# Optimization experiments

Hardware: AMD Instinct MI355X
Metric: run time of the kernel (lower is better)

Reference implementation:

```python
import jax, jax.numpy as jnp
import numpy as np

N = 100000
IN_C = 128
HID = 128
LAT = 64
E = 800000


def gcn_conv(x, src, dst, norm, W, b, num_nodes):
    # x: [N, Cin]; src/dst: [E+N] (self-loops appended); norm: [E+N]
    xw = x @ W                                   # [N, Cout]
    msg = xw[src] * norm[:, None]                # gather + scale, [E+N, Cout]
    out = jax.ops.segment_sum(msg, dst, num_segments=num_nodes)
    return out + b


def setup_inputs() -> dict:
    key = jax.random.key(0)
    ks = jax.random.split(key, 8)
    x = jax.random.normal(ks[0], (N, IN_C), dtype=jnp.float32)
    edge_index = jax.random.randint(ks[1], (2, E), 0, N, dtype=jnp.int64)
    batch = jnp.zeros((N,), dtype=jnp.int64)
    # GCNConv params (Glorot-ish scale)
    W1 = jax.random.normal(ks[2], (IN_C, HID), dtype=jnp.float32) / np.sqrt(IN_C)
    b1 = jnp.zeros((HID,), dtype=jnp.float32)
    Wmu = jax.random.normal(ks[3], (HID, LAT), dtype=jnp.float32) / np.sqrt(HID)
    bmu = jnp.zeros((LAT,), dtype=jnp.float32)
    Wlv = jax.random.normal(ks[4], (HID, LAT), dtype=jnp.float32) / np.sqrt(HID)
    blv = jnp.zeros((LAT,), dtype=jnp.float32)
    return {"x": x, "edge_index": edge_index, "batch": batch,
            "W1": W1, "b1": b1, "Wmu": Wmu, "bmu": bmu, "Wlv": Wlv, "blv": blv}


def reference(x, edge_index, batch, W1, b1, Wmu, bmu, Wlv, blv):
    num_nodes = x.shape[0]
    loop = jnp.arange(num_nodes, dtype=edge_index.dtype)
    src = jnp.concatenate([edge_index[0], loop])   # source nodes (+self loops)
    dst = jnp.concatenate([edge_index[1], loop])   # target nodes (+self loops)
    # symmetric GCN normalization: deg over targets, norm = d[src]^-1/2 * d[dst]^-1/2
    deg = jax.ops.segment_sum(jnp.ones_like(dst, dtype=x.dtype), dst,
                              num_segments=num_nodes)
    dis = jnp.where(deg > 0, jax.lax.rsqrt(deg), 0.0)
    norm = dis[src] * dis[dst]                      # [E+N]

    h = jax.nn.relu(gcn_conv(x, src, dst, norm, W1, b1, num_nodes))
    mu = gcn_conv(h, src, dst, norm, Wmu, bmu, num_nodes)
    logvar = gcn_conv(h, src, dst, norm, Wlv, blv, num_nodes)
    return (mu, logvar)
```

## Files before the change

kernel.cpp:

```cpp
#include <hip/hip_runtime.h>

typedef short bf16x8 __attribute__((ext_vector_type(8)));
typedef float f32x4 __attribute__((ext_vector_type(4)));

#define ELLK 32
#define OCAP 4096
#define CSTRIDE 16

static __device__ __forceinline__ float4 f4zero() { return make_float4(0.f, 0.f, 0.f, 0.f); }

static __device__ __forceinline__ unsigned short f2bf(float f) {
  unsigned u = __float_as_uint(f);
  u += 0x7FFFu + ((u >> 16) & 1u);
  return (unsigned short)(u >> 16);
}
static __device__ __forceinline__ float2 bf2x2(unsigned u) {
  float2 r;
  r.x = __uint_as_float(u << 16);
  r.y = __uint_as_float(u & 0xFFFF0000u);
  return r;
}

__global__ void k_setup(const float* __restrict__ W1, const float* __restrict__ Wmu,
                        const float* __restrict__ Wlv, unsigned short* __restrict__ Wt1,
                        unsigned short* __restrict__ Wt2, uint4* __restrict__ cntz,
                        int* __restrict__ ocount, int nz4, int nbz) {
  int b = blockIdx.x;
  if (b < nbz) {
    int i = b * 256 + threadIdx.x;
    if (i < nz4) cntz[i] = make_uint4(0u, 0u, 0u, 0u);
    if (b == 0 && threadIdx.x == 0) *ocount = 0;
  } else {
    int id = (b - nbz) * 256 + threadIdx.x;
    if (id < 16384) {
      int nn = id >> 7, k = id & 127;
      Wt1[id] = f2bf(W1[k * 128 + nn]);
    } else {
      int id2 = id - 16384;
      int nn = id2 >> 7, k = id2 & 127;
      float v = (nn < 64) ? Wmu[k * 64 + nn] : Wlv[k * 64 + (nn - 64)];
      Wt2[id2] = f2bf(v);
    }
  }
}

__global__ void k_fill(const int* __restrict__ ei, int* __restrict__ cnt,
                       int* __restrict__ ell, int2* __restrict__ ovf,
                       int* __restrict__ ocount, int E, int n) {
  int e = blockIdx.x * 256 + threadIdx.x;
  if (e >= E) return;
  int s = ei[e];
  int d = ei[E + e];
  int pos = atomicAdd(&cnt[(size_t)d * CSTRIDE], 1);
  if (pos < ELLK) {
    ell[(size_t)pos * n + d] = s;
  } else {
    int o = atomicAdd(ocount, 1);
    if (o < OCAP) ovf[o] = make_int2(d, s);
  }
}

__global__ void k_dnorm(const int* __restrict__ cnt, float* __restrict__ dnorm,
                        unsigned* __restrict__ mflag, unsigned* __restrict__ A,
                        unsigned* __restrict__ H, int n) {
  if (blockIdx.x == 0 && threadIdx.x < 128) {
    int t = threadIdx.x;
    if (t < 64) A[(size_t)n * 64 + t] = 0u;
    else        H[(size_t)n * 64 + (t - 64)] = 0u;
  }
  int i = blockIdx.x * 256 + threadIdx.x;
  if (i >= n) return;
  int c = cnt[(size_t)i * CSTRIDE];
  dnorm[i] = rsqrtf((float)(c + 1));
  int m = (c < ELLK) ? c : ELLK;
  mflag[i] = (unsigned)m | ((c > ELLK) ? 0x80000000u : 0u);
}

__global__ __launch_bounds__(256) void k_gemm1(
    const float* __restrict__ x, const unsigned short* __restrict__ Wt,
    const float* __restrict__ dnorm, unsigned short* __restrict__ A, int n) {
  __shared__ unsigned short Wl[128 * 136];
  __shared__ unsigned short Xl[64 * 136];
  const int tid = threadIdx.x;
  const int row0 = blockIdx.x * 64;
  {
    const uint4* Wg = (const uint4*)Wt;
#pragma unroll
    for (int i = 0; i < 8; ++i) {
      int idx = tid + i * 256;
      int r = idx >> 4, c = idx & 15;
      *(uint4*)&Wl[r * 136 + c * 8] = Wg[r * 16 + c];
    }
  }
  {
#pragma unroll
    for (int i = 0; i < 8; ++i) {
      int idx = tid + i * 256;
      int r = idx >> 5, c = idx & 31;
      int gi = row0 + r;
      float4 v = (gi < n) ? ((const float4*)x)[(size_t)gi * 32 + c] : f4zero();
      ushort4 p;
      p.x = f2bf(v.x); p.y = f2bf(v.y); p.z = f2bf(v.z); p.w = f2bf(v.w);
      *(ushort4*)&Xl[r * 136 + c * 4] = p;
    }
  }
  __syncthreads();

  const int wave = tid >> 6, lane = tid & 63;
  const int li = lane & 15, quad = lane >> 4;
  const int m0 = wave * 16;
  f32x4 acc[8];
#pragma unroll
  for (int t = 0; t < 8; ++t) acc[t] = (f32x4){0.f, 0.f, 0.f, 0.f};

#pragma unroll
  for (int kk = 0; kk < 4; ++kk) {
    int ko = kk * 32 + quad * 8;
    bf16x8 a = *(const bf16x8*)&Xl[(m0 + li) * 136 + ko];
#pragma unroll
    for (int nt = 0; nt < 8; ++nt) {
      bf16x8 b = *(const bf16x8*)&Wl[(nt * 16 + li) * 136 + ko];
      acc[nt] = __builtin_amdgcn_mfma_f32_16x16x32_bf16(a, b, acc[nt], 0, 0, 0);
    }
  }
  float dn[4];
#pragma unroll
  for (int r = 0; r < 4; ++r) {
    int gi = row0 + m0 + quad * 4 + r;
    dn[r] = (gi < n) ? dnorm[gi] : 0.f;
  }
  __syncthreads();
#pragma unroll
  for (int nt = 0; nt < 8; ++nt)
#pragma unroll
    for (int r = 0; r < 4; ++r)
      Xl[(m0 + quad * 4 + r) * 136 + nt * 16 + li] = f2bf(acc[nt][r] * dn[r]);
  __syncthreads();
  {
    uint4* A4 = (uint4*)A;
#pragma unroll
    for (int i = 0; i < 4; ++i) {
      int idx = tid + i * 256;
      int r = idx >> 4, c = idx & 15;
      int gi = row0 + r;
      if (gi < n) A4[(size_t)gi * 16 + c] = *(uint4*)&Xl[r * 136 + c * 8];
    }
  }
}

template <bool EPI_RELU>
__global__ __launch_bounds__(256) void k_spmm(
    const unsigned* __restrict__ mflag, const float* __restrict__ dnorm,
    const int* __restrict__ ell, const int2* __restrict__ ovf,
    const int* __restrict__ ocount, const unsigned* __restrict__ S,
    unsigned* __restrict__ D, const float2* __restrict__ bias, int n) {
  int wid = (blockIdx.x * blockDim.x + threadIdx.x) >> 6;
  if (wid >= n) return;
  int lane = threadIdx.x & 63;

  unsigned mf = mflag[wid];
  int m = (int)(mf & 0xFFFFu);
  float dsd = dnorm[wid];
  float2 acc = bf2x2(S[(size_t)wid * 64 + lane]);

  const int* ep = ell + wid;
  int nbt = (m + 7) >> 3;
  for (int b = 0; b < nbt; ++b) {
    int j0 = b * 8;
    int idx[8];
#pragma unroll
    for (int k = 0; k < 8; ++k) idx[k] = ep[(size_t)(j0 + k) * n];
#pragma unroll
    for (int k = 0; k < 8; ++k) idx[k] = (j0 + k < m) ? idx[k] : n;
    unsigned u[8];
#pragma unroll
    for (int k = 0; k < 8; ++k) u[k] = S[(size_t)idx[k] * 64 + lane];
#pragma unroll
    for (int k = 0; k < 8; ++k) {
      float2 f = bf2x2(u[k]);
      acc.x += f.x;
      acc.y += f.y;
    }
  }
  if (mf & 0x80000000u) {
    int oc = *ocount;
    if (oc > OCAP) oc = OCAP;
    for (int k = 0; k < oc; ++k) {
      int2 e = ovf[k];
      if (e.x == wid) {
        float2 u0 = bf2x2(S[(size_t)e.y * 64 + lane]);
        acc.x += u0.x;
        acc.y += u0.y;
      }
    }
  }
  float2 o;
  if (EPI_RELU) {
    float2 b = bias[lane];
    o.x = dsd * fmaxf(fmaf(dsd, acc.x, b.x), 0.f);
    o.y = dsd * fmaxf(fmaf(dsd, acc.y, b.y), 0.f);
  } else {
    o.x = dsd * acc.x;
    o.y = dsd * acc.y;
  }
  unsigned pk = (unsigned)f2bf(o.x) | ((unsigned)f2bf(o.y) << 16);
  D[(size_t)wid * 64 + lane] = pk;
}

__global__ __launch_bounds__(256) void k_gemm2_mfma(
    const unsigned short* __restrict__ G, const unsigned short* __restrict__ Wt,
    const float* __restrict__ bmu, const float* __restrict__ blv,
    float* __restrict__ out, int n) {
  __shared__ unsigned short Wl[128 * 136];
  __shared__ unsigned short Xl[64 * 136];
  const int tid = threadIdx.x;
  const int row0 = blockIdx.x * 64;
  {
    const uint4* Wg = (const uint4*)Wt;
#pragma unroll
    for (int i = 0; i < 8; ++i) {
      int idx = tid + i * 256;
      int r = idx >> 4, c = idx & 15;
      *(uint4*)&Wl[r * 136 + c * 8] = Wg[r * 16 + c];
    }
  }
  {
    const uint4* Gg = (const uint4*)G;
#pragma unroll
    for (int i = 0; i < 4; ++i) {
      int idx = tid + i * 256;
      int r = idx >> 4, c = idx & 15;
      int gi = row0 + r;
      uint4 v = (gi < n) ? Gg[(size_t)gi * 16 + c] : make_uint4(0, 0, 0, 0);
      *(uint4*)&Xl[r * 136 + c * 8] = v;
    }
  }
  __syncthreads();

  const int wave = tid >> 6, lane = tid & 63;
  const int li = lane & 15, quad = lane >> 4;
  const int m0 = wave * 16;

  float bias[8];
#pragma unroll
  for (int nt = 0; nt < 8; ++nt) {
    int c = nt * 16 + li;
    bias[nt] = (c < 64) ? bmu[c] : blv[c - 64];
  }

  f32x4 acc[8];
#pragma unroll
  for (int t = 0; t < 8; ++t) acc[t] = (f32x4){0.f, 0.f, 0.f, 0.f};

#pragma unroll
  for (int kk = 0; kk < 4; ++kk) {
    int ko = kk * 32 + quad * 8;
    bf16x8 a = *(const bf16x8*)&Xl[(m0 + li) * 136 + ko];
#pragma unroll
    for (int nt = 0; nt < 8; ++nt) {
      bf16x8 b = *(const bf16x8*)&Wl[(nt * 16 + li) * 136 + ko];
      acc[nt] = __builtin_amdgcn_mfma_f32_16x16x32_bf16(a, b, acc[nt], 0, 0, 0);
    }
  }
#pragma unroll
  for (int nt = 0; nt < 8; ++nt) {
    int col = nt * 16 + li;
#pragma unroll
    for (int r = 0; r < 4; ++r) {
      int gi = row0 + m0 + quad * 4 + r;
      if (gi < n) {
        float v = acc[nt][r] + bias[nt];
        if (col < 64) out[(size_t)gi * 64 + col] = v;
        else          out[(size_t)(n + gi) * 64 + (col - 64)] = v;
      }
    }
  }
}

extern "C" void kernel_launch(void* const* d_in, const int* in_sizes, int n_in,
                              void* d_out, int out_size, void* d_ws, size_t ws_size,
                              hipStream_t stream) {
  const float* x   = (const float*)d_in[0];
  const int*   ei  = (const int*)d_in[1];
  const float* W1  = (const float*)d_in[3];
  const float* b1  = (const float*)d_in[4];
  const float* Wmu = (const float*)d_in[5];
  const float* bmu = (const float*)d_in[6];
  const float* Wlv = (const float*)d_in[7];
  const float* blv = (const float*)d_in[8];
  float* out = (float*)d_out;

  const int n = in_sizes[0] / 128;
  const int E = in_sizes[1] / 2;

  float* ws = (float*)d_ws;
  size_t p = 0;
  int* cnt    = (int*)(ws + p); p += (size_t)n * CSTRIDE;
  int* ocount = (int*)(ws + p); p += 1;
  p = (p + 3) & ~(size_t)3;
  int* ell    = (int*)(ws + p); p += (size_t)n * ELLK;
  int2* ovf   = (int2*)(ws + p); p += (size_t)OCAP * 2;
  unsigned* A = (unsigned*)(ws + p); p += (size_t)(n + 1) * 64;
  unsigned* H = (unsigned*)(ws + p); p += (size_t)(n + 1) * 64;
  unsigned* G = (unsigned*)(ws + p); p += (size_t)n * 64;
  unsigned short* Wt1 = (unsigned short*)(ws + p); p += 8192;
  unsigned short* Wt2 = (unsigned short*)(ws + p); p += 8192;
  float* dnorm    = (float*)(ws + p); p += n;
  unsigned* mflag = (unsigned*)(ws + p); p += n;

  int nz4  = (n * CSTRIDE) / 4;
  int nbz  = (nz4 + 255) / 256;
  int eb   = (E + 255) / 256;
  int gblk = (n + 63) / 64;
  int nb   = (n + 255) / 256;
  int sblk = (n + 3) / 4;

  k_setup<<<nbz + 128, 256, 0, stream>>>(W1, Wmu, Wlv, Wt1, Wt2, (uint4*)cnt, ocount, nz4, nbz);
  k_fill<<<eb, 256, 0, stream>>>(ei, cnt, ell, ovf, ocount, E, n);
  k_dnorm<<<nb, 256, 0, stream>>>(cnt, dnorm, mflag, A, H, n);
  k_gemm1<<<gblk, 256, 0, stream>>>(x, Wt1, dnorm, (unsigned short*)A, n);
  k_spmm<true><<<sblk, 256, 0, stream>>>(mflag, dnorm, ell, ovf, ocount, A, H,
                                         (const float2*)b1, n);
  k_spmm<false><<<sblk, 256, 0, stream>>>(mflag, dnorm, ell, ovf, ocount, H, G, nullptr, n);
  k_gemm2_mfma<<<gblk, 256, 0, stream>>>((const unsigned short*)G, Wt2, bmu, blv, out, n);
}
```

Before: 298.7 us.

## Split SpMM columns across blocks and batch edge atomics in ELL fill

The SpMM kernel now gives each block 16 nodes and one quarter of the 64 packed columns, with 16 lanes per node instead of a full wavefront. Adjacent blocks therefore cover different column slices of the same nodes, which narrows each gather to a 64-byte segment; the intent is better cache locality and more independent loads per wave. The ELL fill kernel handles four edges per thread and issues their atomics together, and the index loads and ELL stores use nontemporal hints. The risks are that the ELL indices are now re-read four times, once per column slice, and that the 64-byte gathers may use cache lines less efficiently.

```diff
diff --git a/kernel.cpp b/kernel.cpp
--- a/kernel.cpp
+++ b/kernel.cpp
@@ -47,16 +47,28 @@
 __global__ void k_fill(const int* __restrict__ ei, int* __restrict__ cnt,
                        int* __restrict__ ell, int2* __restrict__ ovf,
                        int* __restrict__ ocount, int E, int n) {
-  int e = blockIdx.x * 256 + threadIdx.x;
-  if (e >= E) return;
-  int s = ei[e];
-  int d = ei[E + e];
-  int pos = atomicAdd(&cnt[(size_t)d * CSTRIDE], 1);
-  if (pos < ELLK) {
-    ell[(size_t)pos * n + d] = s;
-  } else {
-    int o = atomicAdd(ocount, 1);
-    if (o < OCAP) ovf[o] = make_int2(d, s);
+  int e0 = blockIdx.x * 1024 + threadIdx.x;
+  int ss[4], dd[4], pos[4];
+  bool ok[4];
+#pragma unroll
+  for (int k = 0; k < 4; ++k) {
+    int e = e0 + k * 256;
+    ok[k] = (e < E);
+    ss[k] = ok[k] ? ei[e] : 0;
+    dd[k] = ok[k] ? ei[E + e] : 0;
+  }
+#pragma unroll
+  for (int k = 0; k < 4; ++k)
+    pos[k] = ok[k] ? atomicAdd(&cnt[(size_t)dd[k] * CSTRIDE], 1) : ELLK;
+#pragma unroll
+  for (int k = 0; k < 4; ++k) {
+    if (!ok[k]) continue;
+    if (pos[k] < ELLK) {
+      __builtin_nontemporal_store(ss[k], &ell[(size_t)pos[k] * n + dd[k]]);
+    } else {
+      int o = atomicAdd(ocount, 1);
+      if (o < OCAP) ovf[o] = make_int2(dd[k], ss[k]);
+    }
   }
 }
 
@@ -154,27 +166,35 @@
     const int* __restrict__ ell, const int2* __restrict__ ovf,
     const int* __restrict__ ocount, const unsigned* __restrict__ S,
     unsigned* __restrict__ D, const float2* __restrict__ bias, int n) {
-  int wid = (blockIdx.x * blockDim.x + threadIdx.x) >> 6;
-  if (wid >= n) return;
-  int lane = threadIdx.x & 63;
-
-  unsigned mf = mflag[wid];
+  const int bid = blockIdx.x;
+  const int s = bid & 3;
+  const int g = bid >> 2;
+  const int tid = threadIdx.x;
+  const int lane = tid & 63;
+  const int nsub = lane >> 4;
+  const int csub = lane & 15;
+  const int node = g * 16 + (tid >> 6) * 4 + nsub;
+  if (node >= n) return;
+  const int col = s * 16 + csub;
+
+  unsigned mf = __builtin_nontemporal_load(&mflag[node]);
   int m = (int)(mf & 0xFFFFu);
-  float dsd = dnorm[wid];
-  float2 acc = bf2x2(S[(size_t)wid * 64 + lane]);
-
-  const int* ep = ell + wid;
+  float dsd = __builtin_nontemporal_load(&dnorm[node]);
+  float2 acc = bf2x2(S[(size_t)node * 64 + col]);
+
+  const int* ep = ell + node;
   int nbt = (m + 7) >> 3;
   for (int b = 0; b < nbt; ++b) {
     int j0 = b * 8;
     int idx[8];
 #pragma unroll
-    for (int k = 0; k < 8; ++k) idx[k] = ep[(size_t)(j0 + k) * n];
+    for (int k = 0; k < 8; ++k)
+      idx[k] = __builtin_nontemporal_load(&ep[(size_t)(j0 + k) * n]);
 #pragma unroll
     for (int k = 0; k < 8; ++k) idx[k] = (j0 + k < m) ? idx[k] : n;
     unsigned u[8];
 #pragma unroll
-    for (int k = 0; k < 8; ++k) u[k] = S[(size_t)idx[k] * 64 + lane];
+    for (int k = 0; k < 8; ++k) u[k] = S[(size_t)idx[k] * 64 + col];
 #pragma unroll
     for (int k = 0; k < 8; ++k) {
       float2 f = bf2x2(u[k]);
@@ -187,8 +207,8 @@
     if (oc > OCAP) oc = OCAP;
     for (int k = 0; k < oc; ++k) {
       int2 e = ovf[k];
-      if (e.x == wid) {
-        float2 u0 = bf2x2(S[(size_t)e.y * 64 + lane]);
+      if (e.x == node) {
+        float2 u0 = bf2x2(S[(size_t)e.y * 64 + col]);
         acc.x += u0.x;
         acc.y += u0.y;
       }
@@ -196,7 +216,7 @@
   }
   float2 o;
   if (EPI_RELU) {
-    float2 b = bias[lane];
+    float2 b = bias[col];
     o.x = dsd * fmaxf(fmaf(dsd, acc.x, b.x), 0.f);
     o.y = dsd * fmaxf(fmaf(dsd, acc.y, b.y), 0.f);
   } else {
@@ -204,7 +224,7 @@
     o.y = dsd * acc.y;
   }
   unsigned pk = (unsigned)f2bf(o.x) | ((unsigned)f2bf(o.y) << 16);
-  D[(size_t)wid * 64 + lane] = pk;
+  D[(size_t)node * 64 + col] = pk;
 }
 
 __global__ __launch_bounds__(256) void k_gemm2_mfma(
@@ -310,10 +330,10 @@
 
   int nz4  = (n * CSTRIDE) / 4;
   int nbz  = (nz4 + 255) / 256;
-  int eb   = (E + 255) / 256;
+  int eb   = (E + 1023) / 1024;
   int gblk = (n + 63) / 64;
   int nb   = (n + 255) / 256;
-  int sblk = (n + 3) / 4;
+  int sblk = ((n + 15) / 16) * 4;
 
   k_setup<<<nbz + 128, 256, 0, stream>>>(W1, Wmu, Wlv, Wt1, Wt2, (uint4*)cnt, ocount, nz4, nbz);
   k_fill<<<eb, 256, 0, stream>>>(ei, cnt, ell, ovf, ocount, E, n);
```

Result: slower. 411.1 us (+37.6%).

## Fuse degree-norm into GEMM1, batch edge fill per thread, widen SpMM gather

Applied to the files above, without the earlier changes.

Removes the separate k_dnorm kernel: the sentinel-row zeroing moves into k_setup, and the degree normalization and mflag computation move into k_gemm1, which shares dnorm through LDS. k_fill now handles four edges per thread, issuing all loads and atomics before the ELL stores and using nontemporal stores. k_spmm unconditionally gathers a first batch of 16 neighbor rows, padding with the zero sentinel row, before looping in batches of 8. This cuts one launch and raises memory-level parallelism, but nodes with few neighbors now issue redundant sentinel loads.

```diff
diff --git a/kernel.cpp b/kernel.cpp
--- a/kernel.cpp
+++ b/kernel.cpp
@@ -24,12 +24,18 @@
 __global__ void k_setup(const float* __restrict__ W1, const float* __restrict__ Wmu,
                         const float* __restrict__ Wlv, unsigned short* __restrict__ Wt1,
                         unsigned short* __restrict__ Wt2, uint4* __restrict__ cntz,
-                        int* __restrict__ ocount, int nz4, int nbz) {
+                        int* __restrict__ ocount, unsigned* __restrict__ A,
+                        unsigned* __restrict__ H, int nz4, int nbz, int n) {
   int b = blockIdx.x;
   if (b < nbz) {
     int i = b * 256 + threadIdx.x;
     if (i < nz4) cntz[i] = make_uint4(0u, 0u, 0u, 0u);
-    if (b == 0 && threadIdx.x == 0) *ocount = 0;
+    if (b == 0) {
+      int t = threadIdx.x;
+      if (t == 0) *ocount = 0;
+      if (t < 64) A[(size_t)n * 64 + t] = 0u;
+      else if (t < 128) H[(size_t)n * 64 + (t - 64)] = 0u;
+    }
   } else {
     int id = (b - nbz) * 256 + threadIdx.x;
     if (id < 16384) {
@@ -47,40 +53,38 @@
 __global__ void k_fill(const int* __restrict__ ei, int* __restrict__ cnt,
                        int* __restrict__ ell, int2* __restrict__ ovf,
                        int* __restrict__ ocount, int E, int n) {
-  int e = blockIdx.x * 256 + threadIdx.x;
-  if (e >= E) return;
-  int s = ei[e];
-  int d = ei[E + e];
-  int pos = atomicAdd(&cnt[(size_t)d * CSTRIDE], 1);
-  if (pos < ELLK) {
-    ell[(size_t)pos * n + d] = s;
-  } else {
-    int o = atomicAdd(ocount, 1);
-    if (o < OCAP) ovf[o] = make_int2(d, s);
-  }
-}
-
-__global__ void k_dnorm(const int* __restrict__ cnt, float* __restrict__ dnorm,
-                        unsigned* __restrict__ mflag, unsigned* __restrict__ A,
-                        unsigned* __restrict__ H, int n) {
-  if (blockIdx.x == 0 && threadIdx.x < 128) {
-    int t = threadIdx.x;
-    if (t < 64) A[(size_t)n * 64 + t] = 0u;
-    else        H[(size_t)n * 64 + (t - 64)] = 0u;
-  }
-  int i = blockIdx.x * 256 + threadIdx.x;
-  if (i >= n) return;
-  int c = cnt[(size_t)i * CSTRIDE];
-  dnorm[i] = rsqrtf((float)(c + 1));
-  int m = (c < ELLK) ? c : ELLK;
-  mflag[i] = (unsigned)m | ((c > ELLK) ? 0x80000000u : 0u);
+  int e0 = blockIdx.x * 1024 + threadIdx.x;
+  int ss[4], dd[4], pos[4];
+  bool ok[4];
+#pragma unroll
+  for (int k = 0; k < 4; ++k) {
+    int e = e0 + k * 256;
+    ok[k] = (e < E);
+    ss[k] = ok[k] ? ei[e] : 0;
+    dd[k] = ok[k] ? ei[E + e] : 0;
+  }
+#pragma unroll
+  for (int k = 0; k < 4; ++k)
+    pos[k] = ok[k] ? atomicAdd(&cnt[(size_t)dd[k] * CSTRIDE], 1) : ELLK;
+#pragma unroll
+  for (int k = 0; k < 4; ++k) {
+    if (!ok[k]) continue;
+    if (pos[k] < ELLK) {
+      __builtin_nontemporal_store(ss[k], &ell[(size_t)pos[k] * n + dd[k]]);
+    } else {
+      int o = atomicAdd(ocount, 1);
+      if (o < OCAP) ovf[o] = make_int2(dd[k], ss[k]);
+    }
+  }
 }
 
 __global__ __launch_bounds__(256) void k_gemm1(
     const float* __restrict__ x, const unsigned short* __restrict__ Wt,
-    const float* __restrict__ dnorm, unsigned short* __restrict__ A, int n) {
+    const int* __restrict__ cnt, unsigned short* __restrict__ A,
+    float* __restrict__ dnorm, unsigned* __restrict__ mflag, int n) {
   __shared__ unsigned short Wl[128 * 136];
   __shared__ unsigned short Xl[64 * 136];
+  __shared__ float dnl[64];
   const int tid = threadIdx.x;
   const int row0 = blockIdx.x * 64;
   {
@@ -106,6 +110,19 @@
   }
   __syncthreads();
 
+  if (tid < 64) {
+    int gi = row0 + tid;
+    float dn = 0.f;
+    if (gi < n) {
+      int c = cnt[(size_t)gi * CSTRIDE];
+      dn = rsqrtf((float)(c + 1));
+      dnorm[gi] = dn;
+      int mm = (c < ELLK) ? c : ELLK;
+      mflag[gi] = (unsigned)mm | ((c > ELLK) ? 0x80000000u : 0u);
+    }
+    dnl[tid] = dn;
+  }
+
   const int wave = tid >> 6, lane = tid & 63;
   const int li = lane & 15, quad = lane >> 4;
   const int m0 = wave * 16;
@@ -123,13 +140,10 @@
       acc[nt] = __builtin_amdgcn_mfma_f32_16x16x32_bf16(a, b, acc[nt], 0, 0, 0);
     }
   }
+  __syncthreads();
   float dn[4];
 #pragma unroll
-  for (int r = 0; r < 4; ++r) {
-    int gi = row0 + m0 + quad * 4 + r;
-    dn[r] = (gi < n) ? dnorm[gi] : 0.f;
-  }
-  __syncthreads();
+  for (int r = 0; r < 4; ++r) dn[r] = dnl[m0 + quad * 4 + r];
 #pragma unroll
   for (int nt = 0; nt < 8; ++nt)
 #pragma unroll
@@ -164,22 +178,38 @@
   float2 acc = bf2x2(S[(size_t)wid * 64 + lane]);
 
   const int* ep = ell + wid;
-  int nbt = (m + 7) >> 3;
-  for (int b = 0; b < nbt; ++b) {
-    int j0 = b * 8;
-    int idx[8];
-#pragma unroll
-    for (int k = 0; k < 8; ++k) idx[k] = ep[(size_t)(j0 + k) * n];
-#pragma unroll
-    for (int k = 0; k < 8; ++k) idx[k] = (j0 + k < m) ? idx[k] : n;
-    unsigned u[8];
-#pragma unroll
-    for (int k = 0; k < 8; ++k) u[k] = S[(size_t)idx[k] * 64 + lane];
-#pragma unroll
-    for (int k = 0; k < 8; ++k) {
+  {
+    int idx[16];
+#pragma unroll
+    for (int k = 0; k < 16; ++k) idx[k] = ep[(size_t)k * n];
+#pragma unroll
+    for (int k = 0; k < 16; ++k) idx[k] = (k < m) ? idx[k] : n;
+    unsigned u[16];
+#pragma unroll
+    for (int k = 0; k < 16; ++k) u[k] = S[(size_t)idx[k] * 64 + lane];
+#pragma unroll
+    for (int k = 0; k < 16; ++k) {
       float2 f = bf2x2(u[k]);
       acc.x += f.x;
       acc.y += f.y;
+    }
+  }
+  if (m > 16) {
+    for (int j0 = 16; j0 < m; j0 += 8) {
+      int idx[8];
+#pragma unroll
+      for (int k = 0; k < 8; ++k) idx[k] = ep[(size_t)(j0 + k) * n];
+#pragma unroll
+      for (int k = 0; k < 8; ++k) idx[k] = (j0 + k < m) ? idx[k] : n;
+      unsigned u[8];
+#pragma unroll
+      for (int k = 0; k < 8; ++k) u[k] = S[(size_t)idx[k] * 64 + lane];
+#pragma unroll
+      for (int k = 0; k < 8; ++k) {
+        float2 f = bf2x2(u[k]);
+        acc.x += f.x;
+        acc.y += f.y;
+      }
     }
   }
   if (mf & 0x80000000u) {
@@ -310,15 +340,14 @@
 
   int nz4  = (n * CSTRIDE) / 4;
   int nbz  = (nz4 + 255) / 256;
-  int eb   = (E + 255) / 256;
+  int eb   = (E + 1023) / 1024;
   int gblk = (n + 63) / 64;
-  int nb   = (n + 255) / 256;
   int sblk = (n + 3) / 4;
 
-  k_setup<<<nbz + 128, 256, 0, stream>>>(W1, Wmu, Wlv, Wt1, Wt2, (uint4*)cnt, ocount, nz4, nbz);
+  k_setup<<<nbz + 128, 256, 0, stream>>>(W1, Wmu, Wlv, Wt1, Wt2, (uint4*)cnt, ocount,
+                                         A, H, nz4, nbz, n);
   k_fill<<<eb, 256, 0, stream>>>(ei, cnt, ell, ovf, ocount, E, n);
-  k_dnorm<<<nb, 256, 0, stream>>>(cnt, dnorm, mflag, A, H, n);
-  k_gemm1<<<gblk, 256, 0, stream>>>(x, Wt1, dnorm, (unsigned short*)A, n);
+  k_gemm1<<<gblk, 256, 0, stream>>>(x, Wt1, cnt, (unsigned short*)A, dnorm, mflag, n);
   k_spmm<true><<<sblk, 256, 0, stream>>>(mflag, dnorm, ell, ovf, ocount, A, H,
                                          (const float2*)b1, n);
   k_spmm<false><<<sblk, 256, 0, stream>>>(mflag, dnorm, ell, ovf, ocount, H, G, nullptr, n);
```

After: 294.9 us. About the same (-1.3%).
